# Performance work log

Measured on AMD Instinct MI355X. Metric: run time of the kernel, lower is better.

The kernel has to match this reference:

```python
import jax, jax.numpy as jnp
import numpy as np
from jax import lax

NUM_HEADS = 8
FOCUSING_FACTOR = 3.0
KERNEL_SIZE = 5


def setup_inputs() -> dict:
    key = jax.random.key(0)
    ks = jax.random.split(key, 9)
    B, C, H, W = 16, 256, 64, 64
    s = 0.02
    return {
        "x": jax.random.normal(ks[0], (B, C, H, W), dtype=jnp.float32),
        "Wq": jax.random.normal(ks[1], (C, C), dtype=jnp.float32) * s,
        "bq": jax.random.normal(ks[2], (C,), dtype=jnp.float32) * s,
        "Wkv": jax.random.normal(ks[3], (2 * C, C), dtype=jnp.float32) * s,
        "bkv": jax.random.normal(ks[4], (2 * C,), dtype=jnp.float32) * s,
        "Wproj": jax.random.normal(ks[5], (C, C), dtype=jnp.float32) * s,
        "bproj": jax.random.normal(ks[6], (C,), dtype=jnp.float32) * s,
        "dwc_w": jax.random.normal(ks[7], (C // NUM_HEADS, 1, KERNEL_SIZE, KERNEL_SIZE), dtype=jnp.float32) * s,
        "dwc_b": jax.random.normal(ks[8], (C // NUM_HEADS,), dtype=jnp.float32) * s,
        "scale_param": jnp.zeros((1, 1, C), dtype=jnp.float32),
    }


def reference(x, Wq, bq, Wkv, bkv, Wproj, bproj, dwc_w, dwc_b, scale_param):
    B, C, H, W = x.shape
    nh = NUM_HEADS
    hd = C // nh
    N = H * W
    num = int(round(N ** 0.5))  # feature map side, N is a perfect square

    xt = x.reshape(B, C, N).transpose(0, 2, 1)  # [B, N, C]
    q = xt @ Wq.T + bq
    kv = xt @ Wkv.T + bkv  # [B, N, 2C] -> (2, C) split on last dim
    k, v = kv[..., :C], kv[..., C:]
    # positional_encoding is freshly-initialized zeros in the original forward -> no-op

    scale = jax.nn.softplus(scale_param)  # [1, 1, C]
    q = (jax.nn.relu(q) + 1e-6) / scale
    k = (jax.nn.relu(k) + 1e-6) / scale
    q_norm = jnp.linalg.norm(q, axis=-1, keepdims=True)
    k_norm = jnp.linalg.norm(k, axis=-1, keepdims=True)
    q = q ** FOCUSING_FACTOR
    k = k ** FOCUSING_FACTOR
    q = q / jnp.linalg.norm(q, axis=-1, keepdims=True) * q_norm
    k = k / jnp.linalg.norm(k, axis=-1, keepdims=True) * k_norm

    def split_heads(t):  # [B, N, C] -> [B*nh, N, hd]
        return t.reshape(B, N, nh, hd).transpose(0, 2, 1, 3).reshape(B * nh, N, hd)

    q, k, v = split_heads(q), split_heads(k), split_heads(v)

    # linear attention (kv path; i*j*(c+d) > c*d*(i+j) for these shapes)
    z = 1.0 / (jnp.einsum('bic,bc->bi', q, k.sum(axis=1)) + 1e-6)  # [BH, N]
    kv_state = jnp.einsum('bjc,bjd->bcd', k, v)  # [BH, hd, hd]
    out = jnp.einsum('bic,bcd->bid', q, kv_state) * z[..., None]  # [BH, N, hd]

    # depthwise conv on v feature map
    fm = v.transpose(0, 2, 1).reshape(B * nh, hd, num, num)
    fm = lax.conv_general_dilated(
        fm, dwc_w, window_strides=(1, 1),
        padding=[(KERNEL_SIZE // 2, KERNEL_SIZE // 2)] * 2,
        dimension_numbers=('NCHW', 'OIHW', 'NCHW'),
        feature_group_count=hd,
    ) + dwc_b[None, :, None, None]
    fm = fm.reshape(B * nh, hd, N).transpose(0, 2, 1)  # [BH, N, hd]

    out = out + fm
    out = out.reshape(B, nh, N, hd).transpose(0, 2, 1, 3).reshape(B, N, C)
    out = out @ Wproj.T + bproj
    return out.transpose(0, 2, 1).reshape(B, C, H, W)
```

## Files before the change

### kernel.cpp

```cpp
#include <hip/hip_runtime.h>
#include <math.h>

#define NB 16
#define NC 256
#define NN 4096
#define HD 32
#define BHD 128
#define KSPLIT 4

typedef unsigned short bf16_t;
typedef __attribute__((ext_vector_type(4))) float floatx4;
typedef __attribute__((ext_vector_type(8))) short shortx8;

__device__ __forceinline__ float bf2f(unsigned int u16) {
  return __uint_as_float(u16 << 16);
}
__device__ __forceinline__ bf16_t f2bf(float f) {
  unsigned int u = __float_as_uint(f);
  return (bf16_t)((u + 0x7FFFu + ((u >> 16) & 1u)) >> 16);
}
__device__ __forceinline__ void bf8_expand(uint4 u, float* f) {
  f[0] = bf2f(u.x & 0xffffu); f[1] = bf2f(u.x >> 16);
  f[2] = bf2f(u.y & 0xffffu); f[3] = bf2f(u.y >> 16);
  f[4] = bf2f(u.z & 0xffffu); f[5] = bf2f(u.z >> 16);
  f[6] = bf2f(u.w & 0xffffu); f[7] = bf2f(u.w >> 16);
}
__device__ __forceinline__ float softplusf(float x) {
  return fmaxf(x, 0.0f) + log1pf(expf(-fabsf(x)));
}

__device__ __forceinline__ void gl_lds16(const void* g, void* l) {
  __builtin_amdgcn_global_load_lds(
      (const __attribute__((address_space(1))) unsigned int*)g,
      (__attribute__((address_space(3))) unsigned int*)l, 16, 0, 0);
}

__global__ __launch_bounds__(256) void k_prepx(
    const float* __restrict__ x, bf16_t* __restrict__ xbf)
{
  __shared__ float T[64][68];
  const int tid = threadIdx.x;
  const int n0 = blockIdx.x * 64, c0 = blockIdx.y * 64, b = blockIdx.z;
  const float* xb = x + (size_t)b * NC * NN;
#pragma unroll
  for (int it = 0; it < 4; ++it) {
    int c = it * 16 + (tid >> 4);
    int n4 = (tid & 15) * 4;
    float4 v = *(const float4*)(xb + (size_t)(c0 + c) * NN + n0 + n4);
    T[c][n4 + 0] = v.x; T[c][n4 + 1] = v.y;
    T[c][n4 + 2] = v.z; T[c][n4 + 3] = v.w;
  }
  __syncthreads();
  bf16_t* ob = xbf + (size_t)b * NN * NC;
#pragma unroll
  for (int it = 0; it < 2; ++it) {
    int n = it * 32 + (tid >> 3);
    int ch = (tid & 7) * 8;
    unsigned short e[8];
#pragma unroll
    for (int j = 0; j < 8; ++j) e[j] = f2bf(T[ch + j][n]);
    uint4 u;
    u.x = e[0] | ((unsigned)e[1] << 16); u.y = e[2] | ((unsigned)e[3] << 16);
    u.z = e[4] | ((unsigned)e[5] << 16); u.w = e[6] | ((unsigned)e[7] << 16);
    *(uint4*)(ob + (size_t)(n0 + n) * NC + c0 + ch) = u;
  }
}

__global__ __launch_bounds__(256) void k_prepw(
    const float* __restrict__ Wq, const float* __restrict__ Wkv,
    const float* __restrict__ Wp, const float* __restrict__ bq,
    const float* __restrict__ bkv, const float* __restrict__ sp,
    bf16_t* __restrict__ Wqkvb, bf16_t* __restrict__ Wpb,
    float* __restrict__ bias768, float* __restrict__ rscale)
{
  const int blk = blockIdx.x;
  const int tid = threadIdx.x;
  if (blk < 768) {
    const float* src = (blk < 256) ? (Wq + (size_t)blk * NC)
                                   : (Wkv + (size_t)(blk - 256) * NC);
    Wqkvb[(size_t)blk * NC + tid] = f2bf(src[tid]);
  } else if (blk < 1024) {
    int j = blk - 768;
    Wpb[(size_t)j * NC + tid] = f2bf(Wp[(size_t)j * NC + tid]);
  } else if (blk == 1024) {
    for (int i = tid; i < 768; i += 256)
      bias768[i] = (i < 256) ? bq[i] : bkv[i - 256];
  } else {
    rscale[tid] = 1.0f / softplusf(sp[tid]);
  }
}

__global__ __launch_bounds__(256) void k_qkv_mfma(
    const bf16_t* __restrict__ xbf, const bf16_t* __restrict__ Wqkvb,
    const float* __restrict__ bias768, bf16_t* __restrict__ qkv)
{
  __shared__ bf16_t As[128 * 32];
  __shared__ bf16_t Bs[128 * 32];
  const int tid = threadIdx.x;
  const int lane = tid & 63;
  const int w = tid >> 6;
  const int b = blockIdx.z;
  const int m0 = blockIdx.x * 128;
  const int n0 = blockIdx.y * 128;
  const bf16_t* Ab = xbf + ((size_t)b * NN + m0) * NC;
  const bf16_t* Bb = Wqkvb + (size_t)n0 * NC;

  const int wm = (w & 1) * 64;
  const int wn = (w >> 1) * 64;
  const int srow = w * 32 + (lane >> 2);
  const int scol = (lane & 3) * 8;
  const int fm = lane & 15;
  const int kg = lane >> 4;

  floatx4 acc[4][4];
#pragma unroll
  for (int i = 0; i < 4; ++i)
#pragma unroll
    for (int j = 0; j < 4; ++j) {
      floatx4 z = {0.f, 0.f, 0.f, 0.f};
      acc[i][j] = z;
    }

  for (int k0 = 0; k0 < NC; k0 += 32) {
#pragma unroll
    for (int r = 0; r < 2; ++r) {
      gl_lds16(Ab + (size_t)(srow + r * 16) * NC + k0 + scol,
               &As[(w * 32 + r * 16) * 32]);
      gl_lds16(Bb + (size_t)(srow + r * 16) * NC + k0 + scol,
               &Bs[(w * 32 + r * 16) * 32]);
    }
    __syncthreads();
    shortx8 af[4], bfg[4];
#pragma unroll
    for (int t = 0; t < 4; ++t) {
      af[t]  = *(const shortx8*)&As[(wm + t * 16 + fm) * 32 + kg * 8];
      bfg[t] = *(const shortx8*)&Bs[(wn + t * 16 + fm) * 32 + kg * 8];
    }
#pragma unroll
    for (int tm = 0; tm < 4; ++tm)
#pragma unroll
      for (int tn = 0; tn < 4; ++tn)
        acc[tm][tn] = __builtin_amdgcn_mfma_f32_16x16x32_bf16(
            af[tm], bfg[tn], acc[tm][tn], 0, 0, 0);
    __syncthreads();
  }

  float bv[4];
#pragma unroll
  for (int tn = 0; tn < 4; ++tn)
    bv[tn] = bias768[n0 + wn + tn * 16 + fm];

  bf16_t* obase = qkv + ((size_t)b * NN + m0) * 768;
#pragma unroll
  for (int tm = 0; tm < 4; ++tm) {
    int mrow = wm + tm * 16 + kg * 4;
#pragma unroll
    for (int tn = 0; tn < 4; ++tn) {
      int n = n0 + wn + tn * 16 + fm;
#pragma unroll
      for (int r = 0; r < 4; ++r)
        obase[(size_t)(mrow + r) * 768 + n] = f2bf(acc[tm][tn][r] + bv[tn]);
    }
  }
}

__global__ __launch_bounds__(256) void k_focus(
    bf16_t* __restrict__ qkv, const float* __restrict__ rscale)
{
  const int lane = threadIdx.x & 63;
  const int w = threadIdx.x >> 6;
  const size_t t = (size_t)blockIdx.x * 4 + w;
  bf16_t* row = qkv + t * 768;
  ushort4 qu = *(ushort4*)(row + lane * 4);
  ushort4 ku = *(ushort4*)(row + 256 + lane * 4);
  float4 s4 = *(const float4*)(rscale + lane * 4);
  float q[4] = {bf2f(qu.x), bf2f(qu.y), bf2f(qu.z), bf2f(qu.w)};
  float k[4] = {bf2f(ku.x), bf2f(ku.y), bf2f(ku.z), bf2f(ku.w)};
  float rs[4] = {s4.x, s4.y, s4.z, s4.w};
  float q3[4], k3[4];
  float sq2 = 0.f, sq6 = 0.f, sk2 = 0.f, sk6 = 0.f;
#pragma unroll
  for (int i = 0; i < 4; ++i) {
    float qi = (fmaxf(q[i], 0.f) + 1e-6f) * rs[i];
    float ki = (fmaxf(k[i], 0.f) + 1e-6f) * rs[i];
    float qc = qi * qi * qi;
    float kc = ki * ki * ki;
    sq2 += qi * qi;  sk2 += ki * ki;
    sq6 += qc * qc;  sk6 += kc * kc;
    q3[i] = qc; k3[i] = kc;
  }
#pragma unroll
  for (int off = 32; off > 0; off >>= 1) {
    sq2 += __shfl_xor(sq2, off);
    sq6 += __shfl_xor(sq6, off);
    sk2 += __shfl_xor(sk2, off);
    sk6 += __shfl_xor(sk6, off);
  }
  float qs = sqrtf(sq2) * rsqrtf(sq6);
  float ks = sqrtf(sk2) * rsqrtf(sk6);
  ushort4 qo, ko;
  qo.x = f2bf(q3[0] * qs); qo.y = f2bf(q3[1] * qs);
  qo.z = f2bf(q3[2] * qs); qo.w = f2bf(q3[3] * qs);
  ko.x = f2bf(k3[0] * ks); ko.y = f2bf(k3[1] * ks);
  ko.z = f2bf(k3[2] * ks); ko.w = f2bf(k3[3] * ks);
  *(ushort4*)(row + lane * 4) = qo;
  *(ushort4*)(row + 256 + lane * 4) = ko;
}

__global__ __launch_bounds__(256) void k_kvstate(
    const bf16_t* __restrict__ qkv, float* __restrict__ kvsp,
    float* __restrict__ ksump)
{
  const int bh = blockIdx.x;
  const int spl = blockIdx.y;
  const int b = bh >> 3, h = bh & 7;
  __shared__ float ks[64][36];
  __shared__ float vs[64][36];
  const int tid = threadIdx.x;
  const int c = tid >> 3;
  const int d4 = (tid & 7) * 4;
  float acc0 = 0.f, acc1 = 0.f, acc2 = 0.f, acc3 = 0.f, ksacc = 0.f;
  const int t0base = spl * (NN / KSPLIT);
  for (int t0 = t0base; t0 < t0base + NN / KSPLIT; t0 += 64) {
#pragma unroll
    for (int r = 0; r < 2; ++r) {
      int idx = r * 256 + tid;
      int tok = idx >> 3;
      int slot = idx & 7;
      const bf16_t* rowp = qkv + ((size_t)b * NN + t0 + tok) * 768 + 256 + h * HD;
      uint4 u;
      float f[8];
      if (slot < 4) {
        u = *(const uint4*)(rowp + slot * 8);
        bf8_expand(u, f);
#pragma unroll
        for (int e = 0; e < 8; ++e) ks[tok][slot * 8 + e] = f[e];
      } else {
        u = *(const uint4*)(rowp + 256 + (slot - 4) * 8);
        bf8_expand(u, f);
#pragma unroll
        for (int e = 0; e < 8; ++e) vs[tok][(slot - 4) * 8 + e] = f[e];
      }
    }
    __syncthreads();
#pragma unroll 4
    for (int t = 0; t < 64; ++t) {
      float kc = ks[t][c];
      float vv[4];
      *(float4*)vv = *(const float4*)&vs[t][d4];
      acc0 += kc * vv[0]; acc1 += kc * vv[1];
      acc2 += kc * vv[2]; acc3 += kc * vv[3];
      ksacc += kc;
    }
    __syncthreads();
  }
  float o[4] = {acc0, acc1, acc2, acc3};
  *(float4*)(kvsp + ((size_t)spl * BHD + bh) * (HD * HD) + c * HD + d4) = *(float4*)o;
  if (d4 == 0) ksump[((size_t)spl * BHD + bh) * HD + c] = ksacc;
}

__global__ __launch_bounds__(256) void k_combine(
    const float* __restrict__ kvsp, const float* __restrict__ ksump,
    float* __restrict__ kvs, float* __restrict__ ksum)
{
  int i = blockIdx.x * 256 + threadIdx.x;
  float v = 0.f;
#pragma unroll
  for (int s = 0; s < KSPLIT; ++s) v += kvsp[(size_t)s * BHD * HD * HD + i];
  kvs[i] = v;
  if (i < BHD * HD) {
    float u = 0.f;
#pragma unroll
    for (int s = 0; s < KSPLIT; ++s) u += ksump[(size_t)s * BHD * HD + i];
    ksum[i] = u;
  }
}

__global__ __launch_bounds__(256) void k_attnout(
    const bf16_t* __restrict__ qkv, const float* __restrict__ kvs,
    const float* __restrict__ ksum, const float* __restrict__ dwc_w,
    const float* __restrict__ dwc_b, bf16_t* __restrict__ attn)
{
  const int bh = blockIdx.z;
  const int b = bh >> 3, h = bh & 7;
  const int y0 = blockIdx.y * 8, x0 = blockIdx.x * 8;
  __shared__ float qt[64][36];
  __shared__ float vt[32][145];
  __shared__ float zt[64];
  const int tid = threadIdx.x;

  {
    int tok = tid >> 2, slot = tid & 3;
    int ty = tok >> 3, tx = tok & 7;
    int n = (y0 + ty) * 64 + (x0 + tx);
    uint4 u = *(const uint4*)(qkv + ((size_t)b * NN + n) * 768 + h * HD + slot * 8);
    float f[8];
    bf8_expand(u, f);
#pragma unroll
    for (int e = 0; e < 8; ++e) qt[tok][slot * 8 + e] = f[e];
  }
  for (int idx = tid; idx < 576; idx += 256) {
    int ht = idx >> 2, slot = idx & 3;
    int hy = y0 + (ht / 12) - 2;
    int hx = x0 + (ht % 12) - 2;
    float f[8] = {0.f, 0.f, 0.f, 0.f, 0.f, 0.f, 0.f, 0.f};
    if (hy >= 0 && hy < 64 && hx >= 0 && hx < 64) {
      int n = hy * 64 + hx;
      uint4 u = *(const uint4*)(qkv + ((size_t)b * NN + n) * 768 + 512 + h * HD + slot * 8);
      bf8_expand(u, f);
    }
#pragma unroll
    for (int e = 0; e < 8; ++e) vt[slot * 8 + e][ht] = f[e];
  }
  __syncthreads();

  if (tid < 64) {
    float dot = 0.f;
#pragma unroll
    for (int c = 0; c < HD; ++c)
      dot += qt[tid][c] * ksum[(size_t)bh * HD + c];
    zt[tid] = 1.f / (dot + 1e-6f);
  }
  __syncthreads();

  const int d = tid & 31;
  const int tg = tid >> 5;
  float kvc[32];
#pragma unroll
  for (int c = 0; c < 32; ++c)
    kvc[c] = kvs[(size_t)bh * (HD * HD) + c * HD + d];
  float wr[25];
#pragma unroll
  for (int j = 0; j < 25; ++j) wr[j] = dwc_w[d * 25 + j];
  const float bd = dwc_b[d];

#pragma unroll
  for (int tt = 0; tt < 8; ++tt) {
    int t = tg * 8 + tt;
    int ty = t >> 3, tx = t & 7;
    float mv = 0.f;
#pragma unroll
    for (int c = 0; c < 32; ++c) mv += qt[t][c] * kvc[c];
    float acc = mv * zt[t] + bd;
#pragma unroll
    for (int ky = 0; ky < 5; ++ky)
#pragma unroll
      for (int kx = 0; kx < 5; ++kx)
        acc += vt[d][(ty + ky) * 12 + (tx + kx)] * wr[ky * 5 + kx];
    int n = (y0 + ty) * 64 + (x0 + tx);
    attn[((size_t)b * NN + n) * NC + h * HD + d] = f2bf(acc);
  }
}

__global__ __launch_bounds__(256) void k_proj_mfma(
    const bf16_t* __restrict__ attn, const bf16_t* __restrict__ Wpb,
    const float* __restrict__ bp, float* __restrict__ out)
{
  __shared__ bf16_t As[128 * 32];
  __shared__ bf16_t Bs[128 * 32];
  const int tid = threadIdx.x;
  const int lane = tid & 63;
  const int w = tid >> 6;
  const size_t m0 = (size_t)blockIdx.x * 128;
  const int n0 = blockIdx.y * 128;
  const bf16_t* Ab = attn + m0 * NC;
  const bf16_t* Bb = Wpb + (size_t)n0 * NC;

  const int wm = (w & 1) * 64;
  const int wn = (w >> 1) * 64;
  const int srow = w * 32 + (lane >> 2);
  const int scol = (lane & 3) * 8;
  const int fm = lane & 15;
  const int kg = lane >> 4;

  floatx4 acc[4][4];
#pragma unroll
  for (int i = 0; i < 4; ++i)
#pragma unroll
    for (int j = 0; j < 4; ++j) {
      floatx4 z = {0.f, 0.f, 0.f, 0.f};
      acc[i][j] = z;
    }

  for (int k0 = 0; k0 < NC; k0 += 32) {
#pragma unroll
    for (int r = 0; r < 2; ++r) {
      gl_lds16(Ab + (size_t)(srow + r * 16) * NC + k0 + scol,
               &As[(w * 32 + r * 16) * 32]);
      gl_lds16(Bb + (size_t)(srow + r * 16) * NC + k0 + scol,
               &Bs[(w * 32 + r * 16) * 32]);
    }
    __syncthreads();
    shortx8 af[4], bfg[4];
#pragma unroll
    for (int t = 0; t < 4; ++t) {
      af[t]  = *(const shortx8*)&As[(wm + t * 16 + fm) * 32 + kg * 8];
      bfg[t] = *(const shortx8*)&Bs[(wn + t * 16 + fm) * 32 + kg * 8];
    }
#pragma unroll
    for (int tm = 0; tm < 4; ++tm)
#pragma unroll
      for (int tn = 0; tn < 4; ++tn)
        acc[tm][tn] = __builtin_amdgcn_mfma_f32_16x16x32_bf16(
            af[tm], bfg[tn], acc[tm][tn], 0, 0, 0);
    __syncthreads();
  }

  const int b = (int)(m0 >> 12);
  const int t0 = (int)(m0 & 4095);
  float* ob = out + (size_t)b * NC * NN;
#pragma unroll
  for (int tn = 0; tn < 4; ++tn) {
    int j = n0 + wn + tn * 16 + fm;
    float bj = bp[j];
#pragma unroll
    for (int tm = 0; tm < 4; ++tm) {
      int trow = t0 + wm + tm * 16 + kg * 4;
      float4 o;
      o.x = acc[tm][tn][0] + bj;
      o.y = acc[tm][tn][1] + bj;
      o.z = acc[tm][tn][2] + bj;
      o.w = acc[tm][tn][3] + bj;
      *(float4*)(ob + (size_t)j * NN + trow) = o;
    }
  }
}

extern "C" void kernel_launch(void* const* d_in, const int* in_sizes, int n_in,
                              void* d_out, int out_size, void* d_ws, size_t ws_size,
                              hipStream_t stream)
{
  (void)in_sizes; (void)n_in; (void)out_size; (void)ws_size;
  const float* x    = (const float*)d_in[0];
  const float* Wq   = (const float*)d_in[1];
  const float* bq   = (const float*)d_in[2];
  const float* Wkv  = (const float*)d_in[3];
  const float* bkv  = (const float*)d_in[4];
  const float* Wp   = (const float*)d_in[5];
  const float* bp   = (const float*)d_in[6];
  const float* dwcw = (const float*)d_in[7];
  const float* dwcb = (const float*)d_in[8];
  const float* sp   = (const float*)d_in[9];
  float* out = (float*)d_out;

  char* wsb = (char*)d_ws;
  bf16_t* qkv  = (bf16_t*)wsb;
  bf16_t* attn = (bf16_t*)(wsb + 100663296u);
  bf16_t* xbf  = attn;
  float*  kvsp = (float*)(wsb + 100663296u + 33554432u);
  float*  ksump = kvsp + (size_t)KSPLIT * BHD * HD * HD;
  float*  kvs   = ksump + (size_t)KSPLIT * BHD * HD;
  float*  ksum  = kvs + (size_t)BHD * HD * HD;
  bf16_t* Wqkvb = (bf16_t*)(ksum + BHD * HD);
  bf16_t* Wpb   = Wqkvb + 768 * 256;
  float*  bias768 = (float*)(Wpb + 256 * 256);
  float*  rscale  = bias768 + 768;

  k_prepx<<<dim3(64, 4, 16), 256, 0, stream>>>(x, xbf);
  k_prepw<<<1026, 256, 0, stream>>>(Wq, Wkv, Wp, bq, bkv, sp, Wqkvb, Wpb, bias768, rscale);
  k_qkv_mfma<<<dim3(32, 6, 16), 256, 0, stream>>>(xbf, Wqkvb, bias768, qkv);
  k_focus<<<16384, 256, 0, stream>>>(qkv, rscale);
  k_kvstate<<<dim3(BHD, KSPLIT), 256, 0, stream>>>(qkv, kvsp, ksump);
  k_combine<<<512, 256, 0, stream>>>(kvsp, ksump, kvs, ksum);
  k_attnout<<<dim3(8, 8, BHD), 256, 0, stream>>>(qkv, kvs, ksum, dwcw, dwcb, attn);
  k_proj_mfma<<<dim3(512, 2), 256, 0, stream>>>(attn, Wpb, bp, out);
}
```

Baseline: 337.5 us.

## Use MFMA for q·kv_state in attnout with row-strip tiles and sliding-window conv

Rewrites the attention-output kernel so each block covers a 4-row strip of 256 tokens and computes q·kv_state and the normaliser q·ksum with bf16 MFMA instructions instead of scalar FMA loops. The depthwise 5x5 conv now reads a bf16 halo stored transposed in shared memory and uses a register sliding window across columns. k_combine now writes kv_state transposed and ksum in bf16 to feed the MFMA operands. The aim is less scalar ALU work and less redundant halo loading, at the cost of extra bf16 rounding of kv_state, ksum and the intermediate q·kv result.

```diff
diff --git a/kernel.cpp b/kernel.cpp
--- a/kernel.cpp
+++ b/kernel.cpp
@@ -261,95 +261,147 @@
 
 __global__ __launch_bounds__(256) void k_combine(
     const float* __restrict__ kvsp, const float* __restrict__ ksump,
-    float* __restrict__ kvs, float* __restrict__ ksum)
-{
-  int i = blockIdx.x * 256 + threadIdx.x;
-  float v = 0.f;
-#pragma unroll
-  for (int s = 0; s < KSPLIT; ++s) v += kvsp[(size_t)s * BHD * HD * HD + i];
-  kvs[i] = v;
-  if (i < BHD * HD) {
+    bf16_t* __restrict__ kvTb, bf16_t* __restrict__ ksumb)
+{
+  const int bh = blockIdx.x;
+  const int tid = threadIdx.x;
+  const int c = tid >> 3;
+  const int d4 = (tid & 7) * 4;
+  float v[4] = {0.f, 0.f, 0.f, 0.f};
+#pragma unroll
+  for (int s = 0; s < KSPLIT; ++s) {
+    const float* p = kvsp + ((size_t)s * BHD + bh) * (HD * HD) + c * HD + d4;
+#pragma unroll
+    for (int e = 0; e < 4; ++e) v[e] += p[e];
+  }
+#pragma unroll
+  for (int e = 0; e < 4; ++e)
+    kvTb[(size_t)bh * (HD * HD) + (d4 + e) * HD + c] = f2bf(v[e]);
+  if (d4 == 0) {
     float u = 0.f;
 #pragma unroll
-    for (int s = 0; s < KSPLIT; ++s) u += ksump[(size_t)s * BHD * HD + i];
-    ksum[i] = u;
-  }
-}
-
+    for (int s = 0; s < KSPLIT; ++s) u += ksump[((size_t)s * BHD + bh) * HD + c];
+    ksumb[(size_t)bh * HD + c] = f2bf(u);
+  }
+}
+
+#define VT_STRIDE 548
 __global__ __launch_bounds__(256) void k_attnout(
-    const bf16_t* __restrict__ qkv, const float* __restrict__ kvs,
-    const float* __restrict__ ksum, const float* __restrict__ dwc_w,
+    const bf16_t* __restrict__ qkv, const bf16_t* __restrict__ kvTb,
+    const bf16_t* __restrict__ ksumb, const float* __restrict__ dwc_w,
     const float* __restrict__ dwc_b, bf16_t* __restrict__ attn)
 {
-  const int bh = blockIdx.z;
+  __shared__ bf16_t vt[32 * VT_STRIDE];
+  __shared__ bf16_t mvz[256 * 32];
+  const int tid = threadIdx.x;
+  const int lane = tid & 63;
+  const int w = tid >> 6;
+  const int s = blockIdx.x;
+  const int bh = blockIdx.y;
   const int b = bh >> 3, h = bh & 7;
-  const int y0 = blockIdx.y * 8, x0 = blockIdx.x * 8;
-  __shared__ float qt[64][36];
-  __shared__ float vt[32][145];
-  __shared__ float zt[64];
-  const int tid = threadIdx.x;
-
-  {
-    int tok = tid >> 2, slot = tid & 3;
-    int ty = tok >> 3, tx = tok & 7;
-    int n = (y0 + ty) * 64 + (x0 + tx);
-    uint4 u = *(const uint4*)(qkv + ((size_t)b * NN + n) * 768 + h * HD + slot * 8);
-    float f[8];
-    bf8_expand(u, f);
-#pragma unroll
-    for (int e = 0; e < 8; ++e) qt[tok][slot * 8 + e] = f[e];
-  }
-  for (int idx = tid; idx < 576; idx += 256) {
-    int ht = idx >> 2, slot = idx & 3;
-    int hy = y0 + (ht / 12) - 2;
-    int hx = x0 + (ht % 12) - 2;
-    float f[8] = {0.f, 0.f, 0.f, 0.f, 0.f, 0.f, 0.f, 0.f};
-    if (hy >= 0 && hy < 64 && hx >= 0 && hx < 64) {
-      int n = hy * 64 + hx;
-      uint4 u = *(const uint4*)(qkv + ((size_t)b * NN + n) * 768 + 512 + h * HD + slot * 8);
-      bf8_expand(u, f);
-    }
-#pragma unroll
-    for (int e = 0; e < 8; ++e) vt[slot * 8 + e][ht] = f[e];
+
+#pragma unroll
+  for (int it = 0; it < 8; ++it) {
+    int idx = it * 256 + tid;
+    int ry = idx >> 8;
+    int col = (idx >> 2) & 63;
+    int slot = idx & 3;
+    int y = s * 4 - 2 + ry;
+    uint4 u = make_uint4(0u, 0u, 0u, 0u);
+    if (y >= 0 && y < 64)
+      u = *(const uint4*)(qkv + ((size_t)b * NN + y * 64 + col) * 768 + 512 + h * HD + slot * 8);
+    unsigned short e[8];
+    e[0] = (unsigned short)(u.x & 0xffffu); e[1] = (unsigned short)(u.x >> 16);
+    e[2] = (unsigned short)(u.y & 0xffffu); e[3] = (unsigned short)(u.y >> 16);
+    e[4] = (unsigned short)(u.z & 0xffffu); e[5] = (unsigned short)(u.z >> 16);
+    e[6] = (unsigned short)(u.w & 0xffffu); e[7] = (unsigned short)(u.w >> 16);
+#pragma unroll
+    for (int j = 0; j < 8; ++j)
+      vt[(slot * 8 + j) * VT_STRIDE + (col + 2) * 8 + ry] = e[j];
+  }
+#pragma unroll
+  for (int e = 0; e < 4; ++e) {
+    int idx = tid * 4 + e;
+    int d = idx >> 5;
+    int rem = idx & 31;
+    int cc4 = rem >> 3;
+    int ry = rem & 7;
+    int cc = (cc4 < 2) ? cc4 : (64 + cc4);
+    vt[d * VT_STRIDE + cc * 8 + ry] = 0;
+  }
+
+  const int fm = lane & 15;
+  const int kg = lane >> 4;
+  shortx8 b0 = *(const shortx8*)(kvTb + (size_t)bh * 1024 + fm * HD + kg * 8);
+  shortx8 b1 = *(const shortx8*)(kvTb + (size_t)bh * 1024 + (16 + fm) * HD + kg * 8);
+  shortx8 b2 = {0, 0, 0, 0, 0, 0, 0, 0};
+  if (fm == 0) b2 = *(const shortx8*)(ksumb + (size_t)bh * HD + kg * 8);
+  floatx4 zf = {0.f, 0.f, 0.f, 0.f};
+#pragma unroll
+  for (int q = 0; q < 4; ++q) {
+    int mt = w * 4 + q;
+    int tok = s * 256 + mt * 16 + fm;
+    shortx8 a = *(const shortx8*)(qkv + ((size_t)b * NN + tok) * 768 + h * HD + kg * 8);
+    floatx4 d0 = __builtin_amdgcn_mfma_f32_16x16x32_bf16(a, b0, zf, 0, 0, 0);
+    floatx4 d1 = __builtin_amdgcn_mfma_f32_16x16x32_bf16(a, b1, zf, 0, 0, 0);
+    floatx4 d2 = __builtin_amdgcn_mfma_f32_16x16x32_bf16(a, b2, zf, 0, 0, 0);
+#pragma unroll
+    for (int r = 0; r < 4; ++r) {
+      float qk = __shfl(d2[r], lane & 48);
+      float z = 1.0f / (qk + 1e-6f);
+      int tl = mt * 16 + kg * 4 + r;
+      mvz[tl * 32 + fm] = f2bf(d0[r] * z);
+      mvz[tl * 32 + 16 + fm] = f2bf(d1[r] * z);
+    }
   }
   __syncthreads();
 
-  if (tid < 64) {
-    float dot = 0.f;
-#pragma unroll
-    for (int c = 0; c < HD; ++c)
-      dot += qt[tid][c] * ksum[(size_t)bh * HD + c];
-    zt[tid] = 1.f / (dot + 1e-6f);
-  }
-  __syncthreads();
-
   const int d = tid & 31;
-  const int tg = tid >> 5;
-  float kvc[32];
-#pragma unroll
-  for (int c = 0; c < 32; ++c)
-    kvc[c] = kvs[(size_t)bh * (HD * HD) + c * HD + d];
+  const int xg = tid >> 5;
+  const int x0c = xg * 8;
   float wr[25];
 #pragma unroll
   for (int j = 0; j < 25; ++j) wr[j] = dwc_w[d * 25 + j];
   const float bd = dwc_b[d];
-
-#pragma unroll
-  for (int tt = 0; tt < 8; ++tt) {
-    int t = tg * 8 + tt;
-    int ty = t >> 3, tx = t & 7;
-    float mv = 0.f;
-#pragma unroll
-    for (int c = 0; c < 32; ++c) mv += qt[t][c] * kvc[c];
-    float acc = mv * zt[t] + bd;
-#pragma unroll
-    for (int ky = 0; ky < 5; ++ky)
-#pragma unroll
-      for (int kx = 0; kx < 5; ++kx)
-        acc += vt[d][(ty + ky) * 12 + (tx + kx)] * wr[ky * 5 + kx];
-    int n = (y0 + ty) * 64 + (x0 + tx);
-    attn[((size_t)b * NN + n) * NC + h * HD + d] = f2bf(acc);
-  }
+  const bf16_t* vd = vt + d * VT_STRIDE;
+
+  float win[5][8];
+#define LOADCOL(dst, cc) do {                                   \
+    const bf16_t* _p = vd + (cc) * 8;                           \
+    uint2 _u0 = *(const uint2*)_p;                              \
+    uint2 _u1 = *(const uint2*)(_p + 4);                        \
+    (dst)[0] = bf2f(_u0.x & 0xffffu); (dst)[1] = bf2f(_u0.x >> 16); \
+    (dst)[2] = bf2f(_u0.y & 0xffffu); (dst)[3] = bf2f(_u0.y >> 16); \
+    (dst)[4] = bf2f(_u1.x & 0xffffu); (dst)[5] = bf2f(_u1.x >> 16); \
+    (dst)[6] = bf2f(_u1.y & 0xffffu); (dst)[7] = bf2f(_u1.y >> 16); \
+  } while (0)
+
+#pragma unroll
+  for (int p = 0; p < 4; ++p) LOADCOL(win[p], x0c + p);
+
+  bf16_t* arow = attn + ((size_t)b * NN + s * 256) * NC + h * HD + d;
+#pragma unroll
+  for (int i = 0; i < 8; ++i) {
+    int x = x0c + i;
+    LOADCOL(win[4], x + 4);
+#pragma unroll
+    for (int ty = 0; ty < 4; ++ty) {
+      float acc = bd;
+#pragma unroll
+      for (int ky = 0; ky < 5; ++ky)
+#pragma unroll
+        for (int kx = 0; kx < 5; ++kx)
+          acc += wr[ky * 5 + kx] * win[kx][ty + ky];
+      int tl = ty * 64 + x;
+      acc += bf2f(mvz[tl * 32 + d]);
+      arow[(size_t)tl * NC] = f2bf(acc);
+    }
+#pragma unroll
+    for (int c2 = 0; c2 < 4; ++c2)
+#pragma unroll
+      for (int r2 = 0; r2 < 8; ++r2) win[c2][r2] = win[c2 + 1][r2];
+  }
+#undef LOADCOL
 }
 
 __global__ __launch_bounds__(256) void k_proj_mfma(
@@ -449,9 +501,9 @@
   bf16_t* xbf  = attn;
   float*  kvsp = (float*)(wsb + 100663296u + 33554432u);
   float*  ksump = kvsp + (size_t)KSPLIT * BHD * HD * HD;
-  float*  kvs   = ksump + (size_t)KSPLIT * BHD * HD;
-  float*  ksum  = kvs + (size_t)BHD * HD * HD;
-  bf16_t* Wqkvb = (bf16_t*)(ksum + BHD * HD);
+  bf16_t* kvTb  = (bf16_t*)(ksump + (size_t)KSPLIT * BHD * HD);
+  bf16_t* ksumb = kvTb + (size_t)BHD * HD * HD;
+  bf16_t* Wqkvb = ksumb + (size_t)BHD * HD;
   bf16_t* Wpb   = Wqkvb + 768 * 256;
   float*  bias768 = (float*)(Wpb + 256 * 256);
   float*  rscale  = bias768 + 768;
@@ -461,7 +513,7 @@
   k_qkv_mfma<<<dim3(32, 6, 16), 256, 0, stream>>>(xbf, Wqkvb, bias768, qkv);
   k_focus<<<16384, 256, 0, stream>>>(qkv, rscale);
   k_kvstate<<<dim3(BHD, KSPLIT), 256, 0, stream>>>(qkv, kvsp, ksump);
-  k_combine<<<512, 256, 0, stream>>>(kvsp, ksump, kvs, ksum);
-  k_attnout<<<dim3(8, 8, BHD), 256, 0, stream>>>(qkv, kvs, ksum, dwcw, dwcb, attn);
+  k_combine<<<BHD, 256, 0, stream>>>(kvsp, ksump, kvTb, ksumb);
+  k_attnout<<<dim3(16, BHD), 256, 0, stream>>>(qkv, kvTb, ksumb, dwcw, dwcb, attn);
   k_proj_mfma<<<dim3(512, 2), 256, 0, stream>>>(attn, Wpb, bp, out);
 }
```

After: 310.8 us. -7.9%, faster.
